# Kernel tuning notes

Hardware: AMD Instinct MI355X
Metric: run time of the kernel (lower is better)

The kernel has to match this reference:

```python
import jax, jax.numpy as jnp
import numpy as np
from jax import lax

K = 9  # propagation kernel

def conv(x, w, b, pad):
    y = lax.conv_general_dilated(x, w, (1, 1), [(pad, pad), (pad, pad)],
                                 dimension_numbers=('NCHW', 'OIHW', 'NCHW'))
    return y + b[None, :, None, None]

def bn(x, g, beta):
    # SynchronizedBatchNorm2d in eval mode with identity running stats (mean=0, var=1)
    return x * g[None, :, None, None] + beta[None, :, None, None]

def propagate(deep, wts):
    # Dynamic local filtering (same math as img2col * weights, sum over 81 taps),
    # computed as 81 shifted-slice FMAs instead of materializing the (n,c,hw,81) tensor.
    p = K // 2
    n, c, h, w = deep.shape
    padded = jnp.pad(deep, ((0, 0), (0, 0), (p, p), (p, p)))
    out = jnp.zeros_like(deep)
    for k in range(K * K):  # k = dy*9 + dx, matching unfold(2).unfold(3) flattening
        dy, dx = k // K, k % K
        out = out + padded[:, :, dy:dy + h, dx:dx + w] * wts[:, k:k + 1]
    return out

def setup_inputs():
    key = jax.random.key(0)
    ks = jax.random.split(key, 40)
    N, C, H, W = 1, 256, 96, 192
    NUM_CLASSES = 19
    s = 0.05
    f32 = jnp.float32
    d = {}
    d['f1_deep'] = jax.random.normal(ks[0], (N, C, H, W), f32)
    d['f1_low'] = jax.random.normal(ks[1], (N, C, H, W), f32)
    d['f2_low'] = jax.random.normal(ks[2], (N, C, H, W), f32)
    # WeightPredictor
    d['wp_c1_w'] = jax.random.normal(ks[3], (256, 256, 3, 3), f32) * s
    d['wp_c1_b'] = jnp.zeros((256,), f32)
    d['wp_c2_w'] = jax.random.normal(ks[4], (256, 512, 3, 3), f32) * s
    d['wp_c2_b'] = jnp.zeros((256,), f32)
    d['wp_fc_w'] = jax.random.normal(ks[5], (81, 256, 1, 1), f32) * s
    d['wp_fc_b'] = jnp.zeros((81,), f32)
    # AdaptiveScheduler
    d['sch_c1_w'] = jax.random.normal(ks[6], (256, 256, 3, 3), f32) * s
    d['sch_c1_b'] = jnp.zeros((256,), f32)
    d['sch_c2_w'] = jax.random.normal(ks[7], (256, 256, 3, 3), f32) * s
    d['sch_c2_b'] = jnp.zeros((256,), f32)
    d['sch_fc_w'] = jax.random.normal(ks[8], (1, 256), f32) * s
    d['sch_fc_b'] = jnp.zeros((1,), f32)
    # AdaptNet
    d['ad_c1_w'] = jax.random.normal(ks[9], (256, 512, 3, 3), f32) * s
    d['ad_c1_b'] = jnp.zeros((256,), f32)
    d['ad_c2_w'] = jax.random.normal(ks[10], (256, 256, 3, 3), f32) * s
    d['ad_c2_b'] = jnp.zeros((256,), f32)
    d['ad_c3_w'] = jax.random.normal(ks[11], (256, 256, 3, 3), f32) * s
    d['ad_c3_b'] = jnp.zeros((256,), f32)
    # reduce_conv2 (1x1 conv + BN)
    d['rc_w'] = jax.random.normal(ks[12], (48, 256, 1, 1), f32) * s
    d['rc_b'] = jnp.zeros((48,), f32)
    d['rc_g'] = jnp.ones((48,), f32)
    d['rc_beta'] = jnp.zeros((48,), f32)
    # last_conv
    d['lc1_w'] = jax.random.normal(ks[13], (256, 304, 3, 3), f32) * s
    d['lc1_b'] = jnp.zeros((256,), f32)
    d['lc1_g'] = jnp.ones((256,), f32)
    d['lc1_beta'] = jnp.zeros((256,), f32)
    d['lc2_w'] = jax.random.normal(ks[14], (256, 256, 3, 3), f32) * s
    d['lc2_b'] = jnp.zeros((256,), f32)
    d['lc2_g'] = jnp.ones((256,), f32)
    d['lc2_beta'] = jnp.zeros((256,), f32)
    d['lc3_w'] = jax.random.normal(ks[15], (NUM_CLASSES, 256, 1, 1), f32) * s
    d['lc3_b'] = jnp.zeros((NUM_CLASSES,), f32)
    return d

def reference(f1_deep, f1_low, f2_low,
              wp_c1_w, wp_c1_b, wp_c2_w, wp_c2_b, wp_fc_w, wp_fc_b,
              sch_c1_w, sch_c1_b, sch_c2_w, sch_c2_b, sch_fc_w, sch_fc_b,
              ad_c1_w, ad_c1_b, ad_c2_w, ad_c2_b, ad_c3_w, ad_c3_b,
              rc_w, rc_b, rc_g, rc_beta,
              lc1_w, lc1_b, lc1_g, lc1_beta,
              lc2_w, lc2_b, lc2_g, lc2_beta,
              lc3_w, lc3_b):
    n, c, h, w = f1_deep.shape
    # WeightPredictor: shared conv1 applied to both low features, cat, conv2, 1x1, softmax over 81 taps
    a1 = conv(f1_low, wp_c1_w, wp_c1_b, 1)
    a2 = conv(f2_low, wp_c1_w, wp_c1_b, 1)
    f = conv(jnp.concatenate([a1, a2], axis=1), wp_c2_w, wp_c2_b, 1)
    kernel = jax.nn.softmax(conv(f, wp_fc_w, wp_fc_b, 0), axis=1)  # (n,81,h,w)
    # AdaptiveScheduler
    diff = conv(f1_low, sch_c1_w, sch_c1_b, 1) - conv(f2_low, sch_c1_w, sch_c1_b, 1)
    o = conv(diff, sch_c2_w, sch_c2_b, 1)
    pooled = jnp.mean(o, axis=(2, 3)).squeeze()  # (256,) since n=1
    deviation = pooled @ sch_fc_w.T + sch_fc_b  # (1,)
    # PropagationModule (dynamic 9x9 local filtering of f1_deep by predicted per-pixel kernel)
    prop = propagate(f1_deep, kernel)  # (n,256,h,w)
    # AdaptNet
    x = conv(jnp.concatenate([f2_low, prop], axis=1), ad_c1_w, ad_c1_b, 1)
    x = conv(x, ad_c2_w, ad_c2_b, 1)
    x = conv(x, ad_c3_w, ad_c3_b, 1)
    # reduce_conv2 + last_conv
    low = bn(conv(f2_low, rc_w, rc_b, 0), rc_g, rc_beta)  # (n,48,h,w)
    x = jnp.concatenate([x, low], axis=1)  # (n,304,h,w)
    x = bn(conv(x, lc1_w, lc1_b, 1), lc1_g, lc1_beta)
    x = bn(conv(x, lc2_w, lc2_b, 1), lc2_g, lc2_beta)
    x = conv(x, lc3_w, lc3_b, 0)  # (n,19,h,w)
    out = jax.image.resize(x, (x.shape[0], x.shape[1], 4 * h, 4 * w), method='bilinear')
    return (out, deviation)
```

## Files before the change

### kernel.cpp

```cpp
#include <hip/hip_runtime.h>
#include <math.h>

#define HWIMG 18432
#define W2 194
#define H2 98
#define NPX1 (H2 * W2)
#define W4 200
#define H4 104
#define NPX4 (H4 * W4)
#define NOUT (19 * 384 * 768)

typedef short bf16x8 __attribute__((ext_vector_type(8)));
typedef float f32x16 __attribute__((ext_vector_type(16)));

__device__ __forceinline__ ushort bf16r(float f) {
    union { float f; unsigned u; } a; a.f = f;
    unsigned u = a.u;
    return (ushort)((u + 0x7fffu + ((u >> 16) & 1u)) >> 16);
}
__device__ __forceinline__ float b2f(ushort u) {
    union { unsigned i; float f; } a; a.i = ((unsigned)u) << 16;
    return a.f;
}
__device__ __forceinline__ bf16x8 ld8(const ushort* p) {
    return *reinterpret_cast<const bf16x8*>(p);
}

__device__ __forceinline__ void gld16(const ushort* g, ushort* l) {
    __builtin_amdgcn_global_load_lds(
        (const __attribute__((address_space(1))) unsigned int*)g,
        (__attribute__((address_space(3))) unsigned int*)l, 16, 0, 0);
}

#define MF(a, b, c) __builtin_amdgcn_mfma_f32_32x32x16_bf16(a, b, c, 0, 0, 0)


__global__ __launch_bounds__(256) void xform_t_k(const float* __restrict__ src,
                                                 const float* __restrict__ src2,
                                                 ushort* __restrict__ dst)
{
    const int px = blockIdx.x * 32 + (threadIdx.x & 31);
    const int c8 = (blockIdx.y * 8 + (threadIdx.x >> 5)) * 8;
    if (px >= NPX1) return;
    const int yP = px / W2, xP = px % W2;
    const int y = yP - 1, x = xP - 1;
    ushort v[8];
    if (y >= 0 && y < 96 && x >= 0 && x < 192) {
        const int p = y * 192 + x;
#pragma unroll
        for (int j = 0; j < 8; ++j) {
            float f = src[(size_t)(c8 + j) * HWIMG + p];
            if (src2) f -= src2[(size_t)(c8 + j) * HWIMG + p];
            v[j] = bf16r(f);
        }
    } else {
#pragma unroll
        for (int j = 0; j < 8; ++j) v[j] = 0;
    }
    *reinterpret_cast<uint4*>(dst + ((size_t)(c8 >> 4) * NPX1 + px) * 16 + (c8 & 15))
        = *reinterpret_cast<uint4*>(v);
}

__global__ __launch_bounds__(256) void xform_nhwc_k(const float* __restrict__ src,
                                                    ushort* __restrict__ dst)
{
    const int px = blockIdx.x * 8 + (threadIdx.x >> 5);
    const int c8 = (threadIdx.x & 31) * 8;
    if (px >= NPX4) return;
    const int yP = px / W4, xP = px % W4;
    const int y = yP - 4, x = xP - 4;
    ushort v[8];
    if (y >= 0 && y < 96 && x >= 0 && x < 192) {
        const int p = y * 192 + x;
#pragma unroll
        for (int j = 0; j < 8; ++j) v[j] = bf16r(src[(size_t)(c8 + j) * HWIMG + p]);
    } else {
#pragma unroll
        for (int j = 0; j < 8; ++j) v[j] = 0;
    }
    *reinterpret_cast<uint4*>(dst + (size_t)px * 256 + c8) = *reinterpret_cast<uint4*>(v);
}

__global__ __launch_bounds__(256) void borderzero3_k(ushort* __restrict__ b0,
                                                     ushort* __restrict__ b1,
                                                     ushort* __restrict__ b2)
{
    ushort* buf = (blockIdx.y == 0) ? b0 : ((blockIdx.y == 1) ? b1 : b2);
    const int idx = blockIdx.x * 256 + threadIdx.x;
    if (idx >= 580 * 16) return;
    const int pi = idx % 580;
    const int cb = idx / 580;
    int pp;
    if (pi < 194) pp = pi;
    else if (pi < 388) pp = 97 * 194 + (pi - 194);
    else if (pi < 484) pp = (pi - 388 + 1) * 194;
    else pp = (pi - 484 + 1) * 194 + 193;
    uint4 z = {0, 0, 0, 0};
    ushort* p = buf + ((size_t)cb * NPX1 + pp) * 16;
    *reinterpret_cast<uint4*>(p) = z;
    *reinterpret_cast<uint4*>(p + 8) = z;
}

struct WtxJob {
    const float* w; const float* b; const float* g; const float* beta;
    int CoutR, Coutp, CinR0, kb0e, CinR1, KBt, ntaps, wtoff, biasoff;
};

__global__ __launch_bounds__(256) void wtx_multi_k(WtxJob J0, WtxJob J1, WtxJob J2,
                                                   WtxJob J3, WtxJob J4, WtxJob J5,
                                                   ushort* __restrict__ wt,
                                                   float* __restrict__ biasout)
{
    WtxJob J = J0;
    switch (blockIdx.y) {
        case 1: J = J1; break; case 2: J = J2; break; case 3: J = J3; break;
        case 4: J = J4; break; case 5: J = J5; break; default: break;
    }
    const int idx = blockIdx.x * 256 + threadIdx.x;
    const int total = J.ntaps * J.KBt * J.Coutp * 16;
    const int CinT = J.CinR0 + J.CinR1;
    if (idx < total) {
        const int c16 = idx & 15;
        const int oc = (idx >> 4) % J.Coutp;
        const int r2 = idx / (16 * J.Coutp);
        const int tap = r2 % J.ntaps;
        const int kbt = r2 / J.ntaps;
        const int k = kbt * 16 + c16;
        float val = 0.f;
        if (oc < J.CoutR) {
            int cit = -1;
            if (k < J.kb0e) { if (k < J.CinR0) cit = k; }
            else { const int k1 = k - J.kb0e; if (k1 < J.CinR1) cit = J.CinR0 + k1; }
            if (cit >= 0) {
                val = J.w[((size_t)oc * CinT + cit) * J.ntaps + tap];
                if (J.g) val *= J.g[oc];
            }
        }
        wt[J.wtoff + idx] = bf16r(val);
    } else if (idx < total + J.Coutp) {
        const int oc = idx - total;
        float v = 0.f;
        if (oc < J.CoutR) {
            v = J.b ? J.b[oc] : 0.f;
            if (J.g) v = v * J.g[oc] + J.beta[oc];
        }
        biasout[J.biasoff + oc] = v;
    }
}

struct ConvJob {
    const ushort* in0; const ushort* in1;
    int KB0, KB1;
    const ushort* wt;
    const float* bias;
    ushort* out;
    int CoutWr;
};

template<int NTAPS>
__global__ __launch_bounds__(256) void conv_lds_k(ConvJob j0, ConvJob j1, ConvJob j2,
                                                  int Coutp)
{
    constexpr int AROWS = (NTAPS == 9) ? 4 : 2;
    constexpr int AW = (NTAPS == 9) ? 66 : 64;
    constexpr int ASLOTS = AROWS * AW * 2;
    __shared__ __align__(16) ushort Abuf[AROWS * AW * 16];
    __shared__ __align__(16) ushort Bbuf[NTAPS * 128 * 16];

    ConvJob J = j0;
    if (blockIdx.y == 1) J = j1;
    else if (blockIdx.y == 2) J = j2;

    const int nblk = gridDim.x;
    const int cpx = nblk >> 3;
    const int sw = ((int)blockIdx.x & 7) * cpx + ((int)blockIdx.x >> 3);
    const int pt = sw % 144;
    const int ocb0 = (sw / 144) * 128;
    const int y0 = (pt / 3) * 2 + 1;
    const int x0 = (pt % 3) * 64 + 1;

    const int tid = threadIdx.x;
    const int lane = tid & 63;
    const int wave = tid >> 6;
    const int wm = wave & 1, wn = wave >> 1;
    const int l31 = lane & 31;
    const int klo8 = (lane >> 5) * 8;

    const int KBtot = J.KB0 + J.KB1;

    f32x16 c00 = {}, c01 = {}, c10 = {}, c11 = {};

    for (int kb = 0; kb < KBtot; ++kb) {
        const ushort* plane = (kb < J.KB0)
            ? (J.in0 + (size_t)kb * (NPX1 * 16))
            : (J.in1 + (size_t)(kb - J.KB0) * (NPX1 * 16));

#pragma unroll
        for (int i = 0; i < (ASLOTS + 255) / 256; ++i) {
            const int f16 = i * 256 + tid;
            if ((ASLOTS % 256 == 0) || (f16 < ASLOTS)) {
                const int e = f16 >> 1;
                const int r = e / AW;
                const int xx = e - r * AW;
                const int px = (NTAPS == 9)
                    ? (y0 - 1 + r) * W2 + (x0 - 1 + xx)
                    : (y0 + r) * W2 + (x0 + xx);
                const ushort* src = plane + (size_t)px * 16 + (f16 & 1) * 8;
                const int wub = (f16 & ~63) * 16;
                gld16(src, (ushort*)((char*)Abuf + __builtin_amdgcn_readfirstlane(wub)));
            }
        }
        {
            const ushort* wsrc = J.wt + ((size_t)kb * NTAPS * Coutp + ocb0) * 16
                               + (size_t)tid * 8;
#pragma unroll
            for (int t = 0; t < NTAPS; ++t) {
                const ushort* src = wsrc + (size_t)t * Coutp * 16;
                const int wub = t * 4096 + (tid & ~63) * 16;
                gld16(src, (ushort*)((char*)Bbuf + __builtin_amdgcn_readfirstlane(wub)));
            }
        }
        __syncthreads();

#pragma unroll
        for (int t = 0; t < NTAPS; ++t) {
            int entA;
            if (NTAPS == 9) entA = (wm + t / 3) * AW + (t % 3) + l31;
            else            entA = wm * 64 + l31;
            bf16x8 a0 = ld8(&Abuf[entA * 16 + klo8]);
            bf16x8 a1 = ld8(&Abuf[(entA + 32) * 16 + klo8]);
            const int entB = t * 128 + wn * 64 + l31;
            bf16x8 b0 = ld8(&Bbuf[entB * 16 + klo8]);
            bf16x8 b1 = ld8(&Bbuf[(entB + 32) * 16 + klo8]);
            c00 = MF(a0, b0, c00);
            c01 = MF(a0, b1, c01);
            c10 = MF(a1, b0, c10);
            c11 = MF(a1, b1, c11);
        }
        __syncthreads();
    }

    const int pxbase = (y0 + wm) * W2 + x0;
    const int rlo = (lane >> 5) * 4;
#pragma unroll
    for (int j = 0; j < 2; ++j) {
        if (ocb0 + wn * 64 + j * 32 + 32 > J.CoutWr) continue;
        const int oc = ocb0 + wn * 64 + j * 32 + l31;
        const float bs = J.bias[oc];
        const size_t obase = (size_t)(oc >> 4) * ((size_t)NPX1 * 16) + (oc & 15);
        const f32x16 v0 = j ? c01 : c00;
        const f32x16 v1 = j ? c11 : c10;
#pragma unroll
        for (int r = 0; r < 16; ++r) {
            const int rw = (r & 3) + 8 * (r >> 2) + rlo;
            J.out[obase + (size_t)(pxbase + rw) * 16] = bf16r(v0[r] + bs);
            J.out[obase + (size_t)(pxbase + 32 + rw) * 16] = bf16r(v1[r] + bs);
        }
    }
}

__global__ __launch_bounds__(256) void softmax81_k(ushort* __restrict__ t)
{
    const int p = blockIdx.x * 256 + threadIdx.x;
    if (p >= HWIMG) return;
    const int y = p / 192, x = p % 192;
    const size_t pp = (size_t)(y + 1) * W2 + (x + 1);
    float v[81];
    float m = -1e30f;
#pragma unroll
    for (int k = 0; k < 81; ++k) {
        v[k] = b2f(t[((size_t)(k >> 4) * NPX1 + pp) * 16 + (k & 15)]);
        m = fmaxf(m, v[k]);
    }
    float s = 0.f;
#pragma unroll
    for (int k = 0; k < 81; ++k) { v[k] = __expf(v[k] - m); s += v[k]; }
    const float inv = 1.f / s;
#pragma unroll
    for (int k = 0; k < 81; ++k)
        t[((size_t)(k >> 4) * NPX1 + pp) * 16 + (k & 15)] = bf16r(v[k] * inv);
}

__global__ __launch_bounds__(256) void prop_k(const ushort* __restrict__ deep,
                                              const ushort* __restrict__ ker,
                                              ushort* __restrict__ out)
{
    __shared__ float kl[8][81];
    const int pxb = blockIdx.x * 8;
    const int t = threadIdx.x;
    for (int i = t; i < 8 * 81; i += 256) {
        const int pp = pxb + i / 81, k = i % 81;
        float kv = 0.f;
        if (pp < NPX1) {
            const int yP = pp / W2, xP = pp % W2;
            if (yP >= 1 && yP <= 96 && xP >= 1 && xP <= 192)
                kv = b2f(ker[((size_t)(k >> 4) * NPX1 + pp) * 16 + (k & 15)]);
        }
        kl[i / 81][k] = kv;
    }
    __syncthreads();
    const int pi = t >> 5;
    const int c8 = (t & 31) * 8;
    const int pp = pxb + pi;
    if (pp >= NPX1) return;
    const int yP = pp / W2, xP = pp % W2;
    ushort* op = out + ((size_t)(c8 >> 4) * NPX1 + pp) * 16 + (c8 & 15);
    if (yP < 1 || yP > 96 || xP < 1 || xP > 192) {
        uint4 z = {0, 0, 0, 0};
        *reinterpret_cast<uint4*>(op) = z;
        return;
    }
    const int y = yP - 1, x = xP - 1;
    float acc[8];
#pragma unroll
    for (int j = 0; j < 8; ++j) acc[j] = 0.f;
    const ushort* dbase = deep + ((size_t)(y + 4) * W4 + (x + 4)) * 256 + c8;
#pragma unroll
    for (int k = 0; k < 81; ++k) {
        const int dy = k / 9 - 4, dx = k % 9 - 4;
        const float kv = kl[pi][k];
        bf16x8 d = ld8(dbase + (ptrdiff_t)(dy * W4 + dx) * 256);
#pragma unroll
        for (int j = 0; j < 8; ++j) acc[j] += b2f((ushort)d[j]) * kv;
    }
    ushort v[8];
#pragma unroll
    for (int j = 0; j < 8; ++j) v[j] = bf16r(acc[j]);
    *reinterpret_cast<uint4*>(op) = *reinterpret_cast<uint4*>(v);
}

__global__ __launch_bounds__(256) void rowsum_k(const ushort* __restrict__ t,
                                                float* __restrict__ partial)
{
    const int y = blockIdx.x, c = threadIdx.x;
    const size_t base = ((size_t)(c >> 4) * NPX1 + (size_t)(y + 1) * W2 + 1) * 16 + (c & 15);
    float s = 0.f;
    for (int x = 0; x < 192; ++x) s += b2f(t[base + (size_t)x * 16]);
    partial[y * 256 + c] = s;
}

__global__ __launch_bounds__(256) void dev_k(const float* __restrict__ partial,
                                             const float* __restrict__ fcw,
                                             const float* __restrict__ fcb,
                                             float* __restrict__ o)
{
    __shared__ float buf[256];
    const int c = threadIdx.x;
    float s = 0.f;
    for (int y = 0; y < 96; ++y) s += partial[y * 256 + c];
    buf[c] = s * fcw[c];
    __syncthreads();
    for (int st = 128; st > 0; st >>= 1) {
        if (c < st) buf[c] += buf[c + st];
        __syncthreads();
    }
    if (c == 0) o[0] = buf[0] * (1.f / (float)HWIMG) + fcb[0];
}

__global__ __launch_bounds__(256) void upsample_k(const ushort* __restrict__ in,
                                                  float* __restrict__ outp)
{
    const int idx = blockIdx.x * 256 + threadIdx.x;
    if (idx >= NOUT) return;
    const int ox = idx % 768;
    const int t = idx / 768;
    const int oy = t % 384;
    const int c = t / 384;

    const float fx = (ox + 0.5f) * 0.25f - 0.5f;
    const float fy = (oy + 0.5f) * 0.25f - 0.5f;
    const int x0 = (int)floorf(fx);
    const int y0 = (int)floorf(fy);
    const float wx = fx - (float)x0;
    const float wy = fy - (float)y0;
    const int x0c = min(max(x0, 0), 191), x1c = min(max(x0 + 1, 0), 191);
    const int y0c = min(max(y0, 0), 95), y1c = min(max(y0 + 1, 0), 95);

    const size_t cb = (size_t)(c >> 4) * NPX1;
    const int c16 = c & 15;
    const float v00 = b2f(in[(cb + (size_t)(y0c + 1) * W2 + (x0c + 1)) * 16 + c16]);
    const float v01 = b2f(in[(cb + (size_t)(y0c + 1) * W2 + (x1c + 1)) * 16 + c16]);
    const float v10 = b2f(in[(cb + (size_t)(y1c + 1) * W2 + (x0c + 1)) * 16 + c16]);
    const float v11 = b2f(in[(cb + (size_t)(y1c + 1) * W2 + (x1c + 1)) * 16 + c16]);
    outp[idx] = (1.f - wy) * ((1.f - wx) * v00 + wx * v01)
              + wy * ((1.f - wx) * v10 + wx * v11);
}

extern "C" void kernel_launch(void* const* d_in, const int* in_sizes, int n_in,
                              void* d_out, int out_size, void* d_ws, size_t ws_size,
                              hipStream_t stream)
{
    const float* f1_deep = (const float*)d_in[0];
    const float* f1_low  = (const float*)d_in[1];
    const float* f2_low  = (const float*)d_in[2];
    const float* wp_c1_w = (const float*)d_in[3];
    const float* wp_c1_b = (const float*)d_in[4];
    const float* wp_c2_w = (const float*)d_in[5];
    const float* wp_c2_b = (const float*)d_in[6];
    const float* wp_fc_w = (const float*)d_in[7];
    const float* wp_fc_b = (const float*)d_in[8];
    const float* sch_c1_w = (const float*)d_in[9];
    const float* sch_c2_w = (const float*)d_in[11];
    const float* sch_c2_b = (const float*)d_in[12];
    const float* sch_fc_w = (const float*)d_in[13];
    const float* sch_fc_b = (const float*)d_in[14];
    const float* ad_c1_w = (const float*)d_in[15];
    const float* ad_c1_b = (const float*)d_in[16];
    const float* ad_c2_w = (const float*)d_in[17];
    const float* ad_c2_b = (const float*)d_in[18];
    const float* ad_c3_w = (const float*)d_in[19];
    const float* ad_c3_b = (const float*)d_in[20];
    const float* rc_w    = (const float*)d_in[21];
    const float* rc_b    = (const float*)d_in[22];
    const float* rc_g    = (const float*)d_in[23];
    const float* rc_beta = (const float*)d_in[24];
    const float* lc1_w   = (const float*)d_in[25];
    const float* lc1_b   = (const float*)d_in[26];
    const float* lc1_g   = (const float*)d_in[27];
    const float* lc1_beta= (const float*)d_in[28];
    const float* lc2_w   = (const float*)d_in[29];
    const float* lc2_b   = (const float*)d_in[30];
    const float* lc2_g   = (const float*)d_in[31];
    const float* lc2_beta= (const float*)d_in[32];
    const float* lc3_w   = (const float*)d_in[33];
    const float* lc3_b   = (const float*)d_in[34];

    float* out = (float*)d_out;
    ushort* ws0 = (ushort*)d_ws;

    const size_t CBBe  = (size_t)NPX1 * 256;
    const size_t BUF0e = (size_t)NPX4 * 256;

    ushort* Bb = ws0 + BUF0e;
    ushort* Cb = Bb + CBBe;
    ushort* Db = Cb + CBBe;
    ushort* Eb = Db + CBBe;
    ushort* Fb = Eb + CBBe;
    ushort* WT = Fb + CBBe;
    float* BIAS = (float*)(WT + 3719168);
    float* PART = BIAS + 12 * 256;
    ushort* L48 = Eb + 6 * (size_t)NPX1 * 16;

    const dim3 b256(256);

    xform_t_k<<<dim3(595, 4), b256, 0, stream>>>(f1_low, nullptr, Bb);
    xform_t_k<<<dim3(595, 4), b256, 0, stream>>>(f2_low, nullptr, Cb);
    xform_t_k<<<dim3(595, 4), b256, 0, stream>>>(f1_low, f2_low, Db);
    borderzero3_k<<<dim3(37, 3), b256, 0, stream>>>(ws0, Eb, Fb);

    {
        WtxJob w0 = {wp_c1_w, wp_c1_b, nullptr, nullptr, 256, 256, 256, 256, 0, 16, 9, 0, 0};
        WtxJob w1 = {sch_c1_w, nullptr, nullptr, nullptr, 256, 256, 256, 256, 0, 16, 9, 589824, 256};
        WtxJob w2 = {wp_c2_w, wp_c2_b, nullptr, nullptr, 256, 256, 256, 256, 256, 32, 9, 1179648, 512};
        WtxJob w3 = {sch_c2_w, sch_c2_b, nullptr, nullptr, 256, 256, 256, 256, 0, 16, 9, 2359296, 768};
        WtxJob w4 = {wp_fc_w, wp_fc_b, nullptr, nullptr, 81, 128, 256, 256, 0, 16, 1, 2949120, 1024};
        WtxJob w5 = {rc_w, rc_b, rc_g, rc_beta, 48, 128, 256, 256, 0, 16, 1, 2981888, 1280};
        wtx_multi_k<<<dim3(4610, 6), b256, 0, stream>>>(w0, w1, w2, w3, w4, w5, WT, BIAS);
    }

    {
        ConvJob a0 = {Bb, Bb, 16, 0, WT, BIAS, Eb, 256};
        ConvJob a1 = {Cb, Cb, 16, 0, WT, BIAS, Fb, 256};
        ConvJob a2 = {Db, Db, 16, 0, WT + 589824, BIAS + 256, ws0, 256};
        conv_lds_k<9><<<dim3(288, 3), b256, 0, stream>>>(a0, a1, a2, 256);
    }
    {
        ConvJob a0 = {Eb, Fb, 16, 16, WT + 1179648, BIAS + 512, Db, 256};
        ConvJob a1 = {ws0, ws0, 16, 0, WT + 2359296, BIAS + 768, Bb, 256};
        conv_lds_k<9><<<dim3(288, 2), b256, 0, stream>>>(a0, a1, a0, 256);
    }
    rowsum_k<<<96, b256, 0, stream>>>(Bb, PART);
    dev_k<<<1, b256, 0, stream>>>(PART, sch_fc_w, sch_fc_b, out + NOUT);

    {
        ConvJob a0 = {Db, Db, 16, 0, WT + 2949120, BIAS + 1024, Eb, 96};
        ConvJob a1 = {Cb, Cb, 16, 0, WT + 2981888, BIAS + 1280, L48, 64};
        conv_lds_k<1><<<dim3(144, 2), b256, 0, stream>>>(a0, a1, a0, 128);
    }

    {
        WtxJob w0 = {ad_c1_w, ad_c1_b, nullptr, nullptr, 256, 256, 256, 256, 256, 32, 9, 0, 1536};
        WtxJob w1 = {ad_c2_w, ad_c2_b, nullptr, nullptr, 256, 256, 256, 256, 0, 16, 9, 1179648, 1792};
        WtxJob w2 = {ad_c3_w, ad_c3_b, nullptr, nullptr, 256, 256, 256, 256, 0, 16, 9, 1769472, 2048};
        WtxJob w3 = {lc1_w, lc1_b, lc1_g, lc1_beta, 256, 256, 256, 256, 48, 20, 9, 2359296, 2304};
        WtxJob w4 = {lc2_w, lc2_b, lc2_g, lc2_beta, 256, 256, 256, 256, 0, 16, 9, 3096576, 2560};
        WtxJob w5 = {lc3_w, lc3_b, nullptr, nullptr, 19, 128, 256, 256, 0, 16, 1, 3686400, 2816};
        wtx_multi_k<<<dim3(4610, 6), b256, 0, stream>>>(w0, w1, w2, w3, w4, w5, WT, BIAS);
    }

    softmax81_k<<<72, b256, 0, stream>>>(Eb);
    xform_nhwc_k<<<2600, b256, 0, stream>>>(f1_deep, ws0);
    prop_k<<<2377, b256, 0, stream>>>(ws0, Eb, Fb);

    {
        ConvJob a = {Cb, Fb, 16, 16, WT, BIAS + 1536, Bb, 256};
        conv_lds_k<9><<<dim3(288, 1), b256, 0, stream>>>(a, a, a, 256);
    }
    {
        ConvJob a = {Bb, Bb, 16, 0, WT + 1179648, BIAS + 1792, Db, 256};
        conv_lds_k<9><<<dim3(288, 1), b256, 0, stream>>>(a, a, a, 256);
    }
    {
        ConvJob a = {Db, Db, 16, 0, WT + 1769472, BIAS + 2048, Fb, 256};
        conv_lds_k<9><<<dim3(288, 1), b256, 0, stream>>>(a, a, a, 256);
    }
    {
        ConvJob a = {Fb, L48, 16, 4, WT + 2359296, BIAS + 2304, Bb, 256};
        conv_lds_k<9><<<dim3(288, 1), b256, 0, stream>>>(a, a, a, 256);
    }
    {
        ConvJob a = {Bb, Bb, 16, 0, WT + 3096576, BIAS + 2560, Db, 256};
        conv_lds_k<9><<<dim3(288, 1), b256, 0, stream>>>(a, a, a, 256);
    }
    {
        ConvJob a = {Db, Db, 16, 0, WT + 3686400, BIAS + 2816, Cb, 32};
        conv_lds_k<1><<<dim3(144, 1), b256, 0, stream>>>(a, a, a, 128);
    }

    upsample_k<<<(NOUT + 255) / 256, b256, 0, stream>>>(Cb, out);
}
```

Baseline: 484.1 us.

## Halve conv block output-channel tile and add XOR-swizzled LDS layout

Each conv block now has 2 waves (128 threads) and covers 64 output channels instead of 128, so the grid doubles. A and B tiles in LDS get an XOR swizzle applied both to the global_load_lds destination mapping and to the MFMA operand reads, aimed at removing LDS bank conflicts. Smaller blocks mean more blocks in flight and better CU fill, but the A tile (input pixels) is now loaded twice as often per output channel, which costs extra global/L2 traffic.

```diff
diff --git a/kernel.cpp b/kernel.cpp
--- a/kernel.cpp
+++ b/kernel.cpp
@@ -33,6 +33,8 @@
 }
 
 #define MF(a, b, c) __builtin_amdgcn_mfma_f32_32x32x16_bf16(a, b, c, 0, 0, 0)
+
+__device__ __forceinline__ int swz(int L) { return L ^ (((L >> 7) & 7) << 4); }
 
 
 __global__ __launch_bounds__(256) void xform_t_k(const float* __restrict__ src,
@@ -158,14 +160,14 @@
 };
 
 template<int NTAPS>
-__global__ __launch_bounds__(256) void conv_lds_k(ConvJob j0, ConvJob j1, ConvJob j2,
+__global__ __launch_bounds__(128) void conv_lds_k(ConvJob j0, ConvJob j1, ConvJob j2,
                                                   int Coutp)
 {
     constexpr int AROWS = (NTAPS == 9) ? 4 : 2;
     constexpr int AW = (NTAPS == 9) ? 66 : 64;
     constexpr int ASLOTS = AROWS * AW * 2;
-    __shared__ __align__(16) ushort Abuf[AROWS * AW * 16];
-    __shared__ __align__(16) ushort Bbuf[NTAPS * 128 * 16];
+    __shared__ __align__(128) ushort Abuf[AROWS * AW * 16];
+    __shared__ __align__(128) ushort Bbuf[NTAPS * 64 * 16];
 
     ConvJob J = j0;
     if (blockIdx.y == 1) J = j1;
@@ -175,16 +177,19 @@
     const int cpx = nblk >> 3;
     const int sw = ((int)blockIdx.x & 7) * cpx + ((int)blockIdx.x >> 3);
     const int pt = sw % 144;
-    const int ocb0 = (sw / 144) * 128;
+    const int ocb0 = (sw / 144) * 64;
     const int y0 = (pt / 3) * 2 + 1;
     const int x0 = (pt % 3) * 64 + 1;
 
     const int tid = threadIdx.x;
     const int lane = tid & 63;
-    const int wave = tid >> 6;
-    const int wm = wave & 1, wn = wave >> 1;
+    const int wm = tid >> 6;
     const int l31 = lane & 31;
-    const int klo8 = (lane >> 5) * 8;
+    const int h16 = (lane >> 5) * 16;
+
+    const int bl = swz(tid * 16);
+    const int b_r = bl >> 5;
+    const int b_h8 = ((bl >> 4) & 1) * 8;
 
     const int KBtot = J.KB0 + J.KB1;
 
@@ -196,27 +201,28 @@
             : (J.in1 + (size_t)(kb - J.KB0) * (NPX1 * 16));
 
 #pragma unroll
-        for (int i = 0; i < (ASLOTS + 255) / 256; ++i) {
-            const int f16 = i * 256 + tid;
-            if ((ASLOTS % 256 == 0) || (f16 < ASLOTS)) {
-                const int e = f16 >> 1;
+        for (int i = 0; i < (ASLOTS + 127) / 128; ++i) {
+            const int f16 = i * 128 + tid;
+            if ((ASLOTS % 128 == 0) || (f16 < ASLOTS)) {
+                const int L = swz(f16 * 16);
+                const int e = L >> 5;
+                const int h8 = ((L >> 4) & 1) * 8;
                 const int r = e / AW;
                 const int xx = e - r * AW;
                 const int px = (NTAPS == 9)
                     ? (y0 - 1 + r) * W2 + (x0 - 1 + xx)
                     : (y0 + r) * W2 + (x0 + xx);
-                const ushort* src = plane + (size_t)px * 16 + (f16 & 1) * 8;
+                const ushort* src = plane + (size_t)px * 16 + h8;
                 const int wub = (f16 & ~63) * 16;
                 gld16(src, (ushort*)((char*)Abuf + __builtin_amdgcn_readfirstlane(wub)));
             }
         }
         {
-            const ushort* wsrc = J.wt + ((size_t)kb * NTAPS * Coutp + ocb0) * 16
-                               + (size_t)tid * 8;
+            const ushort* wsrc = J.wt + ((size_t)kb * NTAPS * Coutp + ocb0 + b_r) * 16 + b_h8;
 #pragma unroll
             for (int t = 0; t < NTAPS; ++t) {
                 const ushort* src = wsrc + (size_t)t * Coutp * 16;
-                const int wub = t * 4096 + (tid & ~63) * 16;
+                const int wub = t * 2048 + (tid & ~63) * 16;
                 gld16(src, (ushort*)((char*)Bbuf + __builtin_amdgcn_readfirstlane(wub)));
             }
         }
@@ -227,11 +233,12 @@
             int entA;
             if (NTAPS == 9) entA = (wm + t / 3) * AW + (t % 3) + l31;
             else            entA = wm * 64 + l31;
-            bf16x8 a0 = ld8(&Abuf[entA * 16 + klo8]);
-            bf16x8 a1 = ld8(&Abuf[(entA + 32) * 16 + klo8]);
-            const int entB = t * 128 + wn * 64 + l31;
-            bf16x8 b0 = ld8(&Bbuf[entB * 16 + klo8]);
-            bf16x8 b1 = ld8(&Bbuf[(entB + 32) * 16 + klo8]);
+            const int SA = swz(entA * 32 + h16);
+            bf16x8 a0 = ld8((const ushort*)((const char*)Abuf + SA));
+            bf16x8 a1 = ld8((const ushort*)((const char*)Abuf + SA + 1024));
+            const int SB = swz((t * 64 + l31) * 32 + h16);
+            bf16x8 b0 = ld8((const ushort*)((const char*)Bbuf + SB));
+            bf16x8 b1 = ld8((const ushort*)((const char*)Bbuf + SB + 1024));
             c00 = MF(a0, b0, c00);
             c01 = MF(a0, b1, c01);
             c10 = MF(a1, b0, c10);
@@ -244,8 +251,8 @@
     const int rlo = (lane >> 5) * 4;
 #pragma unroll
     for (int j = 0; j < 2; ++j) {
-        if (ocb0 + wn * 64 + j * 32 + 32 > J.CoutWr) continue;
-        const int oc = ocb0 + wn * 64 + j * 32 + l31;
+        if (ocb0 + j * 32 + 32 > J.CoutWr) continue;
+        const int oc = ocb0 + j * 32 + l31;
         const float bs = J.bias[oc];
         const size_t obase = (size_t)(oc >> 4) * ((size_t)NPX1 * 16) + (oc & 15);
         const f32x16 v0 = j ? c01 : c00;
@@ -441,7 +448,7 @@
     float* PART = BIAS + 12 * 256;
     ushort* L48 = Eb + 6 * (size_t)NPX1 * 16;
 
-    const dim3 b256(256);
+    const dim3 b256(256), b128(128);
 
     xform_t_k<<<dim3(595, 4), b256, 0, stream>>>(f1_low, nullptr, Bb);
     xform_t_k<<<dim3(595, 4), b256, 0, stream>>>(f2_low, nullptr, Cb);
@@ -462,12 +469,12 @@
         ConvJob a0 = {Bb, Bb, 16, 0, WT, BIAS, Eb, 256};
         ConvJob a1 = {Cb, Cb, 16, 0, WT, BIAS, Fb, 256};
         ConvJob a2 = {Db, Db, 16, 0, WT + 589824, BIAS + 256, ws0, 256};
-        conv_lds_k<9><<<dim3(288, 3), b256, 0, stream>>>(a0, a1, a2, 256);
+        conv_lds_k<9><<<dim3(576, 3), b128, 0, stream>>>(a0, a1, a2, 256);
     }
     {
         ConvJob a0 = {Eb, Fb, 16, 16, WT + 1179648, BIAS + 512, Db, 256};
         ConvJob a1 = {ws0, ws0, 16, 0, WT + 2359296, BIAS + 768, Bb, 256};
-        conv_lds_k<9><<<dim3(288, 2), b256, 0, stream>>>(a0, a1, a0, 256);
+        conv_lds_k<9><<<dim3(576, 2), b128, 0, stream>>>(a0, a1, a0, 256);
     }
     rowsum_k<<<96, b256, 0, stream>>>(Bb, PART);
     dev_k<<<1, b256, 0, stream>>>(PART, sch_fc_w, sch_fc_b, out + NOUT);
@@ -475,7 +482,7 @@
     {
         ConvJob a0 = {Db, Db, 16, 0, WT + 2949120, BIAS + 1024, Eb, 96};
         ConvJob a1 = {Cb, Cb, 16, 0, WT + 2981888, BIAS + 1280, L48, 64};
-        conv_lds_k<1><<<dim3(144, 2), b256, 0, stream>>>(a0, a1, a0, 128);
+        conv_lds_k<1><<<dim3(288, 2), b128, 0, stream>>>(a0, a1, a0, 128);
     }
 
     {
@@ -494,27 +501,27 @@
 
     {
         ConvJob a = {Cb, Fb, 16, 16, WT, BIAS + 1536, Bb, 256};
-        conv_lds_k<9><<<dim3(288, 1), b256, 0, stream>>>(a, a, a, 256);
+        conv_lds_k<9><<<dim3(576, 1), b128, 0, stream>>>(a, a, a, 256);
     }
     {
         ConvJob a = {Bb, Bb, 16, 0, WT + 1179648, BIAS + 1792, Db, 256};
-        conv_lds_k<9><<<dim3(288, 1), b256, 0, stream>>>(a, a, a, 256);
+        conv_lds_k<9><<<dim3(576, 1), b128, 0, stream>>>(a, a, a, 256);
     }
     {
         ConvJob a = {Db, Db, 16, 0, WT + 1769472, BIAS + 2048, Fb, 256};
-        conv_lds_k<9><<<dim3(288, 1), b256, 0, stream>>>(a, a, a, 256);
+        conv_lds_k<9><<<dim3(576, 1), b128, 0, stream>>>(a, a, a, 256);
     }
     {
         ConvJob a = {Fb, L48, 16, 4, WT + 2359296, BIAS + 2304, Bb, 256};
-        conv_lds_k<9><<<dim3(288, 1), b256, 0, stream>>>(a, a, a, 256);
+        conv_lds_k<9><<<dim3(576, 1), b128, 0, stream>>>(a, a, a, 256);
     }
     {
         ConvJob a = {Bb, Bb, 16, 0, WT + 3096576, BIAS + 2560, Db, 256};
-        conv_lds_k<9><<<dim3(288, 1), b256, 0, stream>>>(a, a, a, 256);
+        conv_lds_k<9><<<dim3(576, 1), b128, 0, stream>>>(a, a, a, 256);
     }
     {
         ConvJob a = {Db, Db, 16, 0, WT + 3686400, BIAS + 2816, Cb, 32};
-        conv_lds_k<1><<<dim3(144, 1), b256, 0, stream>>>(a, a, a, 128);
+        conv_lds_k<1><<<dim3(288, 1), b128, 0, stream>>>(a, a, a, 128);
     }
 
     upsample_k<<<(NOUT + 255) / 256, b256, 0, stream>>>(Cb, out);
```

After: 510.5 us. 1.05x slower.
